# Kernel tuning notes

Hardware: AMD Instinct MI355X
Metric: run time of the kernel (lower is better)

## Reference

```python
import jax, jax.numpy as jnp
import numpy as np

B, L, E = 2, 2048, 1024
H = 16
DH = E // H  # head dim for qk and v (dim_qk=dim_v=embed_dim)
HID = 4 * E  # fcn_dim_factor * dim_v
SCALE = DH ** 0.5


def setup_inputs() -> dict:
    key = jax.random.key(0)
    ks = jax.random.split(key, 12)
    s = lambda fan_in: 1.0 / np.sqrt(fan_in)
    return {
        "x": jax.random.uniform(ks[0], (B, L), jnp.float32),
        "z": jax.random.normal(ks[1], (B, L, E), jnp.float32),
        "Wq": jax.random.normal(ks[2], (E, E), jnp.float32) * s(E),
        "bq": jnp.zeros((E,), jnp.float32),
        "Wk": jax.random.normal(ks[3], (E, E), jnp.float32) * s(E),
        "bk": jnp.zeros((E,), jnp.float32),
        "Wv": jax.random.normal(ks[4], (E, E), jnp.float32) * s(E),
        "bv": jnp.zeros((E,), jnp.float32),
        "W1": jax.random.normal(ks[5], (E, HID), jnp.float32) * s(E),
        "b1": jnp.zeros((HID,), jnp.float32),
        "W2": jax.random.normal(ks[6], (HID, 1), jnp.float32) * s(HID),
        "b2": jnp.zeros((1,), jnp.float32),
    }


def reference(x, z, Wq, bq, Wk, bk, Wv, bv, W1, b1, W2, b2):
    # Projections -> (B, H, L, DH)
    def heads(t):
        return t.reshape(B, L, H, DH).transpose(0, 2, 1, 3)

    Q = heads(z @ Wq + bq)
    K = heads(z @ Wk + bk)
    V = heads(z @ Wv + bv)

    # Scores (B, H, L, L)
    S = jnp.einsum("bhid,bhjd->bhij", Q, K) / SCALE

    # Weighted softmax along query axis (dim=-2), weighted by population x
    w = x[:, None, :, None]  # (B, 1, L, 1), broadcasts over queries i
    m = jnp.max(S, axis=-2, keepdims=True)
    e = w * jnp.exp(S - m)
    A = e / jnp.sum(e, axis=-2, keepdims=True)

    # V scaled by population weight, then AV
    V_scaled = w * V
    O = jnp.einsum("bhij,bhjd->bhid", A, V_scaled)  # (B, H, L, DH)
    O = O.transpose(0, 2, 1, 3).reshape(B, L, H * DH)

    # FFN: Linear -> GELU (exact) -> Linear(->1) -> squeeze
    y = jax.nn.gelu(O @ W1 + b1, approximate=False)
    y = (y @ W2 + b2).squeeze(-1)  # (B, L)
    return y
```

## Files before the change

### kernel.cpp

```cpp
#include <hip/hip_runtime.h>
#include <hip/hip_bf16.h>
#include <math.h>

#define B_    2
#define L_    2048
#define E_    1024
#define H_    16
#define DH_   64
#define HID_  4096
#define NROW_ (B_*L_)
#define BH_   (B_*H_)

#define QSCL  0.18033688011112042f

typedef __attribute__((ext_vector_type(8)))  short    short8v;
typedef _Float16 half8v __attribute__((ext_vector_type(8)));
typedef __attribute__((ext_vector_type(16))) float    f32x16;

#define MFMA32(A, Bv, C) __builtin_amdgcn_mfma_f32_32x32x16_bf16((A), (Bv), (C), 0, 0, 0)
#define MFMAH(A, Bv, C)  __builtin_amdgcn_mfma_f32_32x32x16_f16((A), (Bv), (C), 0, 0, 0)

#define WAITV(N) asm volatile("s_waitcnt vmcnt(" #N ")" ::: "memory")
#define SBAR()   __builtin_amdgcn_s_barrier()

__device__ __forceinline__ unsigned short f2bf(float f) {
    union { float f; unsigned u; } v; v.f = f;
    return (unsigned short)((v.u + 0x8000u) >> 16);
}
__device__ __forceinline__ unsigned pack2_bf16(float lo, float hi) {
    union { float f; unsigned u; } a, b; a.f = lo; b.f = hi;
    return __builtin_amdgcn_perm(b.u + 0x8000u, a.u + 0x8000u, 0x07060302u);
}
__device__ __forceinline__ float bf2f(unsigned short u) {
    union { unsigned u; float f; } v; v.u = ((unsigned)u) << 16;
    return v.f;
}

__device__ __forceinline__ void gl_lds16(const void* g, void* l) {
    __builtin_amdgcn_global_load_lds(
        (const __attribute__((address_space(1))) unsigned int*)g,
        (__attribute__((address_space(3))) unsigned int*)l, 16, 0, 0);
}

__device__ __forceinline__ float erf_fast(float v) {
    float a = fabsf(v);
    float t = __builtin_amdgcn_rcpf(1.0f + 0.3275911f * a);
    float p = t * (0.254829592f + t * (-0.284496736f + t * (1.421413741f +
              t * (-1.453152027f + t * 1.061405429f))));
    float r = 1.0f - p * __expf(-a * a);
    return copysignf(r, v);
}

__global__ __launch_bounds__(256) void zh_prep(
    const float* __restrict__ z, _Float16* __restrict__ zh)
{
    const size_t i = ((size_t)blockIdx.x * 256 + threadIdx.x) * 8;
    float4 a = *(const float4*)&z[i];
    float4 b = *(const float4*)&z[i + 4];
    union { _Float16 h[8]; half8v v; } o;
    o.h[0] = (_Float16)a.x; o.h[1] = (_Float16)a.y;
    o.h[2] = (_Float16)a.z; o.h[3] = (_Float16)a.w;
    o.h[4] = (_Float16)b.x; o.h[5] = (_Float16)b.y;
    o.h[6] = (_Float16)b.z; o.h[7] = (_Float16)b.w;
    *(half8v*)&zh[i] = o.v;
}

__global__ __launch_bounds__(256) void wprep3(
    const float* __restrict__ Wq, const float* __restrict__ Wk,
    const float* __restrict__ Wv,
    _Float16* __restrict__ Tq, _Float16* __restrict__ Tk,
    _Float16* __restrict__ Tv)
{
    const float* src = (blockIdx.z == 0) ? Wq : (blockIdx.z == 1) ? Wk : Wv;
    _Float16*    dst = (blockIdx.z == 0) ? Tq : (blockIdx.z == 1) ? Tk : Tv;
    __shared__ float tile[64][65];
    const int t  = threadIdx.x;
    const int r0 = blockIdx.y * 64, c0 = blockIdx.x * 64;
    #pragma unroll
    for (int u = 0; u < 4; ++u) {
        int f = t + 256 * u, row = f >> 4, c4 = (f & 15) << 2;
        *(float4*)&tile[row][c4] = *(const float4*)&src[(size_t)(r0 + row) * E_ + c0 + c4];
    }
    __syncthreads();
    #pragma unroll
    for (int u = 0; u < 4; ++u) {
        int f = t + 256 * u, c = f >> 4, r4 = (f & 15) << 2;
        union { _Float16 h[4]; uint2 u2; } pk;
        pk.h[0] = (_Float16)tile[r4 + 0][c];
        pk.h[1] = (_Float16)tile[r4 + 1][c];
        pk.h[2] = (_Float16)tile[r4 + 2][c];
        pk.h[3] = (_Float16)tile[r4 + 3][c];
        *(uint2*)&dst[(size_t)(c0 + c) * E_ + r0 + r4] = pk.u2;
    }
}

__global__ __launch_bounds__(256) void w1prep(
    const float* __restrict__ W1, _Float16* __restrict__ W1t)
{
    __shared__ float tile[64][65];
    const int t  = threadIdx.x;
    const int r0 = blockIdx.y * 64, c0 = blockIdx.x * 64;
    #pragma unroll
    for (int u = 0; u < 4; ++u) {
        int f = t + 256 * u, row = f >> 4, c4 = (f & 15) << 2;
        *(float4*)&tile[row][c4] = *(const float4*)&W1[(size_t)(r0 + row) * HID_ + c0 + c4];
    }
    __syncthreads();
    #pragma unroll
    for (int u = 0; u < 4; ++u) {
        int f = t + 256 * u, c = f >> 4, r4 = (f & 15) << 2;
        union { _Float16 h[4]; uint2 u2; } pk;
        pk.h[0] = (_Float16)tile[r4 + 0][c];
        pk.h[1] = (_Float16)tile[r4 + 1][c];
        pk.h[2] = (_Float16)tile[r4 + 2][c];
        pk.h[3] = (_Float16)tile[r4 + 3][c];
        *(uint2*)&W1t[(size_t)(c0 + c) * E_ + r0 + r4] = pk.u2;
    }
}

__global__ __launch_bounds__(256) void qkv_mfma(
    const _Float16* __restrict__ zh,
    const _Float16* __restrict__ Tall,
    const float* __restrict__ bq, const float* __restrict__ bk,
    const float* __restrict__ bv,
    unsigned short* __restrict__ outQKV)
{
    const int which = blockIdx.y >> 3;
    const float* bias = (which == 0) ? bq : (which == 1) ? bk : bv;
    const float  osc  = (which == 0) ? QSCL : 1.0f;
    unsigned short* out = outQKV + (size_t)which * ((size_t)BH_ * L_ * DH_);

    __shared__ _Float16 Ah[2][128 * 64];
    __shared__ _Float16 Bs[2][128 * 64];

    const int t    = threadIdx.x;
    const int lane = t & 63;
    const int w    = t >> 6;
    const int l31  = lane & 31;
    const int hq   = lane >> 5;
    const int wm   = w >> 1, wn = w & 1;
    const int m0   = blockIdx.x * 128;
    const int n0   = blockIdx.y * 128;

    const int srow0 = (lane >> 3);
    const int ssl   = lane & 7;

    f32x16 acc[2][2] = {};

#define QKV_STAGE(bb, kc)                                                          \
    {                                                                              \
        _Pragma("unroll")                                                          \
        for (int u = 0; u < 4; ++u) {                                              \
            int ch  = w * 4 + u;                                                   \
            int row = ch * 8 + srow0;                                              \
            gl_lds16(&zh[(size_t)(m0 + row) * E_ + (kc) * 64 + ((ssl ^ (row & 7)) << 3)], \
                     &Ah[bb][ch * 512]);                                           \
            gl_lds16(&Tall[(size_t)(n0 + row) * E_ + (kc) * 64 + ((ssl ^ (row & 7)) << 3)], \
                     &Bs[bb][ch * 512]);                                           \
        }                                                                          \
    }

    QKV_STAGE(0, 0);
    QKV_STAGE(1, 1);
    __syncthreads();
    int cur = 0;

    for (int kc = 0; kc < 16; ++kc) {
        if (kc < 15) WAITV(8); else WAITV(0);
        SBAR();
        __builtin_amdgcn_s_setprio(1);
        #pragma unroll
        for (int ks = 0; ks < 4; ++ks) {
            half8v fb[2];
            #pragma unroll
            for (int nb = 0; nb < 2; ++nb) {
                int br = wn * 64 + nb * 32 + l31;
                fb[nb] = *(const half8v*)&Bs[cur][br * 64 + (((ks * 2 + hq) ^ (br & 7)) << 3)];
            }
            #pragma unroll
            for (int mb = 0; mb < 2; ++mb) {
                int ar = wm * 64 + mb * 32 + l31;
                half8v fa = *(const half8v*)&Ah[cur][ar * 64 + (((ks * 2 + hq) ^ (ar & 7)) << 3)];
                acc[mb][0] = MFMAH(fa, fb[0], acc[mb][0]);
                acc[mb][1] = MFMAH(fa, fb[1], acc[mb][1]);
            }
        }
        __builtin_amdgcn_s_setprio(0);
        SBAR();
        if (kc + 2 < 16) QKV_STAGE(cur, kc + 2);
        cur ^= 1;
    }

    #pragma unroll
    for (int nb = 0; nb < 2; ++nb) {
        int n  = n0 + wn * 64 + nb * 32 + l31;
        int nn = n & 1023;
        int h  = nn >> 6, dh = nn & 63;
        float bb = bias[nn];
        #pragma unroll
        for (int mb = 0; mb < 2; ++mb) {
            #pragma unroll
            for (int r = 0; r < 16; ++r) {
                int m  = m0 + wm * 64 + mb * 32 + (r & 3) + 8 * (r >> 2) + 4 * hq;
                int b  = m >> 11, i = m & (L_ - 1);
                out[((size_t)(b * H_ + h) * L_ + i) * DH_ + dh] = f2bf((acc[mb][nb][r] + bb) * osc);
            }
        }
    }
#undef QKV_STAGE
}

__global__ __launch_bounds__(512) void col_stats_mfma(
    const unsigned short* __restrict__ Qb, const unsigned short* __restrict__ Kb,
    const float* __restrict__ x, float* __restrict__ Do)
{
    __shared__ unsigned short Qlds[2][2][128 * 64];
    __shared__ float xlds[L_];
    __shared__ float cD[4][64];

    const int t    = threadIdx.x;
    const int lane = t & 63;
    const int wv   = t >> 6;
    const int jwv  = wv & 3;
    const int ih   = wv >> 2;
    const int l31  = lane & 31;
    const int hq   = lane >> 5;
    const int bh   = blockIdx.y;
    const int b    = bh >> 4;
    const int j0   = blockIdx.x * 256 + jwv * 64;

    const int srow0 = (lane >> 3);
    const int ssl   = lane & 7;

    {
        *(float4*)&xlds[t * 4] = *(const float4*)&x[(size_t)b * L_ + t * 4];
    }

    short8v kf[2][4];
    #pragma unroll
    for (int s = 0; s < 2; ++s) {
        const unsigned short* kp = Kb + ((size_t)bh * L_ + j0 + s * 32 + l31) * DH_ + hq * 8;
        #pragma unroll
        for (int c = 0; c < 4; ++c) kf[s][c] = *(const short8v*)(kp + c * 16);
    }

    float d0[16], d1[16];
    #pragma unroll
    for (int r = 0; r < 16; ++r) { d0[r] = 0.f; d1[r] = 0.f; }

#define CS_STAGE(bb, lt)                                                            \
    {                                                                               \
        _Pragma("unroll")                                                           \
        for (int u = 0; u < 4; ++u) {                                               \
            int ch  = jwv * 4 + u;                                                  \
            int row = ch * 8 + srow0;                                               \
            gl_lds16(&Qb[((size_t)bh * L_ + (size_t)(ih * 8 + (lt)) * 128 + row) * DH_ + ((ssl ^ (row & 7)) << 3)], \
                     &Qlds[ih][bb][ch * 512]);                                      \
        }                                                                           \
    }

    CS_STAGE(0, 0);
    CS_STAGE(1, 1);
    __syncthreads();
    int cur = 0;

    for (int lt = 0; lt < 8; ++lt) {
        if (lt < 7) WAITV(4); else WAITV(0);
        SBAR();
        #pragma unroll
        for (int cc = 0; cc < 4; ++cc) {
            f32x16 a0 = {}, a1 = {};
            __builtin_amdgcn_s_setprio(1);
            #pragma unroll
            for (int c = 0; c < 4; ++c) {
                int qr = cc * 32 + l31;
                short8v qv = *(const short8v*)&Qlds[ih][cur][qr * 64 + (((c * 2 + hq) ^ (qr & 7)) << 3)];
                a0 = MFMA32(kf[0][c], qv, a0);
                a1 = MFMA32(kf[1][c], qv, a1);
            }
            __builtin_amdgcn_s_setprio(0);
            float xi = xlds[(ih * 8 + lt) * 128 + cc * 32 + l31];
            #pragma unroll
            for (int r = 0; r < 16; ++r) {
                d0[r] += xi * __builtin_amdgcn_exp2f(a0[r]);
                d1[r] += xi * __builtin_amdgcn_exp2f(a1[r]);
            }
        }
        SBAR();
        if (lt + 2 < 8) CS_STAGE(cur, lt + 2);
        cur ^= 1;
    }

    #pragma unroll
    for (int r = 0; r < 16; ++r) {
        #pragma unroll
        for (int off = 16; off > 0; off >>= 1) {
            d0[r] += __shfl_xor(d0[r], off);
            d1[r] += __shfl_xor(d1[r], off);
        }
    }
    if (ih == 1 && l31 == 0) {
        #pragma unroll
        for (int r = 0; r < 16; ++r) {
            int jr = 4 * hq + (r & 3) + 8 * (r >> 2);
            cD[jwv][jr]      = d0[r];
            cD[jwv][32 + jr] = d1[r];
        }
    }
    __syncthreads();
    if (ih == 0 && l31 == 0) {
        #pragma unroll
        for (int r = 0; r < 16; ++r) {
            int jr = 4 * hq + (r & 3) + 8 * (r >> 2);
            Do[(size_t)bh * L_ + j0 + jr]      = d0[r] + cD[jwv][jr];
            Do[(size_t)bh * L_ + j0 + 32 + jr] = d1[r] + cD[jwv][32 + jr];
        }
    }
#undef CS_STAGE
}

__global__ __launch_bounds__(256) void vt_prep(
    const unsigned short* __restrict__ Vb, const float* __restrict__ x,
    const float* __restrict__ Do, unsigned short* __restrict__ Vt)
{
    __shared__ float sc[64];
    __shared__ unsigned short vt[64][66];

    const int t  = threadIdx.x;
    const int bh = blockIdx.y;
    const int b  = bh >> 4;
    const int j0 = blockIdx.x * 64;

    if (t < 64) {
        int j = j0 + t;
        sc[t] = x[(size_t)b * L_ + j] / Do[(size_t)bh * L_ + j];
    }
    __syncthreads();

    #pragma unroll
    for (int u = 0; u < 2; ++u) {
        int idx = t + 256 * u;
        int row = idx >> 3, off = (idx & 7) * 8;
        short8v v = *(const short8v*)&Vb[((size_t)bh * L_ + j0 + row) * DH_ + off];
        float s = sc[row];
        const unsigned short* vs = (const unsigned short*)&v;
        #pragma unroll
        for (int k = 0; k < 8; ++k)
            vt[row][off + k] = f2bf(bf2f(vs[k]) * s);
    }
    __syncthreads();

    #pragma unroll
    for (int u = 0; u < 2; ++u) {
        int idx = t + 256 * u;
        int dh = idx >> 3, js = (idx & 7) * 8;
        unsigned short o[8];
        #pragma unroll
        for (int k = 0; k < 8; ++k) o[k] = vt[js + k][dh];
        *(short8v*)&Vt[((size_t)bh * DH_ + dh) * L_ + j0 + js] = *(const short8v*)o;
    }
}

__global__ __launch_bounds__(512) void attn_out_mfma(
    const unsigned short* __restrict__ Qb, const unsigned short* __restrict__ Kb,
    const unsigned short* __restrict__ Vt, const float* __restrict__ x,
    _Float16* __restrict__ Of)
{
    __shared__ unsigned short Klds[2][2][64 * 64];
    __shared__ unsigned short Vlds[2][2][64 * 64];
    __shared__ float comb[4][64 * 67];

    const int t    = threadIdx.x;
    const int lane = t & 63;
    const int wv   = t >> 6;
    const int iwv  = wv & 3;
    const int jh   = wv >> 2;
    const int l31  = lane & 31;
    const int hq   = lane >> 5;
    const int bh   = blockIdx.y;
    const int b    = bh >> 4, hh = bh & 15;
    const int iw   = blockIdx.x * 256 + iwv * 64;

    const int srow0 = (lane >> 3);
    const int ssl   = lane & 7;

    short8v qf[2][4];
    #pragma unroll
    for (int ig = 0; ig < 2; ++ig) {
        const unsigned short* qp = Qb + ((size_t)bh * L_ + iw + ig * 32 + l31) * DH_ + hq * 8;
        #pragma unroll
        for (int c = 0; c < 4; ++c) qf[ig][c] = *(const short8v*)(qp + c * 16);
    }

    f32x16 accO[2][2] = {};

#define AO_STAGE(bb, jt)                                                            \
    {                                                                               \
        _Pragma("unroll")                                                           \
        for (int u = 0; u < 2; ++u) {                                               \
            int ch  = iwv * 2 + u;                                                  \
            int row = ch * 8 + srow0;                                               \
            gl_lds16(&Kb[((size_t)bh * L_ + (jt) * 64 + row) * DH_ + ((ssl ^ (row & 7)) << 3)], \
                     &Klds[jh][bb][ch * 512]);                                      \
            gl_lds16(&Vt[((size_t)bh * DH_ + row) * L_ + (jt) * 64 + ((ssl ^ (row & 7)) << 3)], \
                     &Vlds[jh][bb][ch * 512]);                                      \
        }                                                                           \
    }

    AO_STAGE(0, jh * 16 + 0);
    AO_STAGE(1, jh * 16 + 1);
    __syncthreads();
    int cur = 0;

    for (int ltj = 0; ltj < 16; ++ltj) {
        if (ltj < 15) WAITV(4); else WAITV(0);
        SBAR();

        uint4 pa[2][4];
        #pragma unroll
        for (int js = 0; js < 2; ++js) {
            f32x16 as0 = {}, as1 = {};
            __builtin_amdgcn_s_setprio(1);
            #pragma unroll
            for (int c = 0; c < 4; ++c) {
                int krow = js * 32 + l31;
                short8v kfr = *(const short8v*)&Klds[jh][cur][krow * 64 + (((c * 2 + hq) ^ (krow & 7)) << 3)];
                as0 = MFMA32(kfr, qf[0][c], as0);
                as1 = MFMA32(kfr, qf[1][c], as1);
            }
            __builtin_amdgcn_s_setprio(0);
            #pragma unroll
            for (int ig = 0; ig < 2; ++ig) {
                const f32x16& as = (ig == 0) ? as0 : as1;
                float p[16];
                #pragma unroll
                for (int r = 0; r < 16; ++r) p[r] = __builtin_amdgcn_exp2f(as[r]);

                unsigned P0 = pack2_bf16(p[0], p[1]);
                unsigned P1 = pack2_bf16(p[2], p[3]);
                unsigned Q0 = pack2_bf16(p[4], p[5]);
                unsigned Q1 = pack2_bf16(p[6], p[7]);
                asm("v_permlane32_swap_b32 %0, %1" : "+v"(P0), "+v"(Q0));
                asm("v_permlane32_swap_b32 %0, %1" : "+v"(P1), "+v"(Q1));
                pa[ig][js * 2 + 0] = make_uint4(P0, P1, Q0, Q1);

                unsigned R0 = pack2_bf16(p[8],  p[9]);
                unsigned R1 = pack2_bf16(p[10], p[11]);
                unsigned S0 = pack2_bf16(p[12], p[13]);
                unsigned S1 = pack2_bf16(p[14], p[15]);
                asm("v_permlane32_swap_b32 %0, %1" : "+v"(R0), "+v"(S0));
                asm("v_permlane32_swap_b32 %0, %1" : "+v"(R1), "+v"(S1));
                pa[ig][js * 2 + 1] = make_uint4(R0, R1, S0, S1);
            }
        }

        __builtin_amdgcn_s_setprio(1);
        #pragma unroll
        for (int c = 0; c < 4; ++c) {
            union { uint4 u; short8v s; } pa0, pa1;
            pa0.u = pa[0][c]; pa1.u = pa[1][c];
            int r0 = l31, r1 = 32 + l31;
            short8v vf0 = *(const short8v*)&Vlds[jh][cur][r0 * 64 + (((c * 2 + hq) ^ (r0 & 7)) << 3)];
            short8v vf1 = *(const short8v*)&Vlds[jh][cur][r1 * 64 + (((c * 2 + hq) ^ (r1 & 7)) << 3)];
            accO[0][0] = MFMA32(pa0.s, vf0, accO[0][0]);
            accO[0][1] = MFMA32(pa0.s, vf1, accO[0][1]);
            accO[1][0] = MFMA32(pa1.s, vf0, accO[1][0]);
            accO[1][1] = MFMA32(pa1.s, vf1, accO[1][1]);
        }
        __builtin_amdgcn_s_setprio(0);
        SBAR();
        if (ltj + 2 < 16) AO_STAGE(cur, jh * 16 + ltj + 2);
        cur ^= 1;
    }

    if (jh == 1) {
        float* cb = &comb[iwv][lane * 67];
        #pragma unroll
        for (int g = 0; g < 2; ++g)
            #pragma unroll
            for (int h = 0; h < 2; ++h)
                #pragma unroll
                for (int r = 0; r < 16; ++r)
                    cb[(g * 2 + h) * 16 + r] = accO[g][h][r];
    }
    __syncthreads();
    if (jh == 0) {
        const float* cb = &comb[iwv][lane * 67];
        #pragma unroll
        for (int g = 0; g < 2; ++g)
            #pragma unroll
            for (int h = 0; h < 2; ++h)
                #pragma unroll
                for (int r = 0; r < 16; ++r)
                    accO[g][h][r] += cb[(g * 2 + h) * 16 + r];

        #pragma unroll
        for (int ig = 0; ig < 2; ++ig) {
            #pragma unroll
            for (int q = 0; q < 4; ++q) {
                float4 xq = *(const float4*)&x[(size_t)b * L_ + iw + ig * 32 + 4 * hq + 8 * q];
                const float xs[4] = { xq.x, xq.y, xq.z, xq.w };
                #pragma unroll
                for (int k = 0; k < 4; ++k) {
                    int r    = q * 4 + k;
                    int irow = iw + ig * 32 + 4 * hq + 8 * q + k;
                    size_t base = ((size_t)b * L_ + irow) * E_ + hh * DH_;
                    Of[base + l31]      = (_Float16)(accO[ig][0][r] * xs[k]);
                    Of[base + 32 + l31] = (_Float16)(accO[ig][1][r] * xs[k]);
                }
            }
        }
    }
#undef AO_STAGE
}

__global__ __launch_bounds__(256) void mlp_mfma(
    const _Float16* __restrict__ Of, const _Float16* __restrict__ W1t,
    const float* __restrict__ b1, const float* __restrict__ W2,
    const float* __restrict__ b2, float* __restrict__ y)
{
    __shared__ _Float16 Oh[2][128 * 64];
    __shared__ _Float16 Wh[2][128 * 64];

    const int t    = threadIdx.x;
    const int lane = t & 63;
    const int w    = t >> 6;
    const int l31  = lane & 31;
    const int hq   = lane >> 5;
    const int wm   = w >> 1, wn = w & 1;
    const int m0   = blockIdx.x * 128;
    const int n0   = blockIdx.y * 128;

    const int srow0 = (lane >> 3);
    const int ssl   = lane & 7;

    f32x16 acc[2][2] = {};

#define MLP_STAGE(bb, kc)                                                          \
    {                                                                              \
        _Pragma("unroll")                                                          \
        for (int u = 0; u < 4; ++u) {                                              \
            int ch  = w * 4 + u;                                                   \
            int row = ch * 8 + srow0;                                              \
            gl_lds16(&Of[(size_t)(m0 + row) * E_ + (kc) * 64 + ((ssl ^ (row & 7)) << 3)], \
                     &Oh[bb][ch * 512]);                                           \
            gl_lds16(&W1t[(size_t)(n0 + row) * E_ + (kc) * 64 + ((ssl ^ (row & 7)) << 3)], \
                     &Wh[bb][ch * 512]);                                           \
        }                                                                          \
    }

    MLP_STAGE(0, 0);
    MLP_STAGE(1, 1);
    __syncthreads();
    int cur = 0;

    for (int kc = 0; kc < 16; ++kc) {
        if (kc < 15) WAITV(8); else WAITV(0);
        SBAR();
        __builtin_amdgcn_s_setprio(1);
        #pragma unroll
        for (int ks = 0; ks < 4; ++ks) {
            half8v fb[2];
            #pragma unroll
            for (int nb = 0; nb < 2; ++nb) {
                int br = wn * 64 + nb * 32 + l31;
                fb[nb] = *(const half8v*)&Wh[cur][br * 64 + (((ks * 2 + hq) ^ (br & 7)) << 3)];
            }
            #pragma unroll
            for (int mb = 0; mb < 2; ++mb) {
                int ar = wm * 64 + mb * 32 + l31;
                half8v fa = *(const half8v*)&Oh[cur][ar * 64 + (((ks * 2 + hq) ^ (ar & 7)) << 3)];
                acc[mb][0] = MFMAH(fa, fb[0], acc[mb][0]);
                acc[mb][1] = MFMAH(fa, fb[1], acc[mb][1]);
            }
        }
        __builtin_amdgcn_s_setprio(0);
        SBAR();
        if (kc + 2 < 16) MLP_STAGE(cur, kc + 2);
        cur ^= 1;
    }

    const int hid0 = n0 + wn * 64 + l31;
    const float bb0 = b1[hid0],      w20 = W2[hid0];
    const float bb1 = b1[hid0 + 32], w21 = W2[hid0 + 32];
    const float b2v = (blockIdx.y == 0) ? b2[0] : 0.0f;
    #pragma unroll
    for (int mb = 0; mb < 2; ++mb) {
        #pragma unroll
        for (int r = 0; r < 16; ++r) {
            float h0 = acc[mb][0][r] + bb0;
            float h1 = acc[mb][1][r] + bb1;
            float s  = 0.5f * h0 * (1.0f + erf_fast(h0 * 0.70710678f)) * w20
                     + 0.5f * h1 * (1.0f + erf_fast(h1 * 0.70710678f)) * w21;
            #pragma unroll
            for (int off = 16; off > 0; off >>= 1) s += __shfl_xor(s, off);
            if (l31 == 0) {
                int m = m0 + wm * 64 + mb * 32 + (r & 3) + 8 * (r >> 2) + 4 * hq;
                atomicAdd(&y[m], s + b2v);
            }
        }
    }
#undef MLP_STAGE
}

extern "C" void kernel_launch(void* const* d_in, const int* in_sizes, int n_in,
                              void* d_out, int out_size, void* d_ws, size_t ws_size,
                              hipStream_t stream)
{
    const float* x  = (const float*)d_in[0];
    const float* z  = (const float*)d_in[1];
    const float* Wq = (const float*)d_in[2];
    const float* bq = (const float*)d_in[3];
    const float* Wk = (const float*)d_in[4];
    const float* bk = (const float*)d_in[5];
    const float* Wv = (const float*)d_in[6];
    const float* bv = (const float*)d_in[7];
    const float* W1 = (const float*)d_in[8];
    const float* b1 = (const float*)d_in[9];
    const float* W2 = (const float*)d_in[10];
    const float* b2 = (const float*)d_in[11];
    float* y = (float*)d_out;

    const size_t NQ = (size_t)BH_ * L_ * DH_;
    unsigned short* p = (unsigned short*)d_ws;
    unsigned short* Qb  = p;  p += NQ;
    unsigned short* Kb  = p;  p += NQ;
    unsigned short* Vb  = p;  p += NQ;
    unsigned short* Vt  = p;  p += NQ;
    _Float16* zh  = (_Float16*)p;  p += (size_t)NROW_ * E_;
    _Float16* Tq  = (_Float16*)p;  p += (size_t)E_ * E_;
    _Float16* Tk  = (_Float16*)p;  p += (size_t)E_ * E_;
    _Float16* Tv  = (_Float16*)p;  p += (size_t)E_ * E_;
    _Float16* W1t = (_Float16*)p;  p += (size_t)HID_ * E_;
    _Float16* Ofp = (_Float16*)p;  p += (size_t)NROW_ * E_;
    float* Dw = (float*)p;

    hipMemsetAsync(y, 0, (size_t)out_size * sizeof(float), stream);

    zh_prep<<<dim3((NROW_ * E_) / (256 * 8)), 256, 0, stream>>>(z, zh);
    wprep3 <<<dim3(E_ / 64, E_ / 64, 3), 256, 0, stream>>>(Wq, Wk, Wv, Tq, Tk, Tv);
    w1prep <<<dim3(HID_ / 64, E_ / 64), 256, 0, stream>>>(W1, W1t);

    qkv_mfma<<<dim3(NROW_ / 128, 3 * E_ / 128), 256, 0, stream>>>(
        zh, Tq, bq, bk, bv, Qb);

    col_stats_mfma<<<dim3(L_ / 256, BH_), 512, 0, stream>>>(Qb, Kb, x, Dw);

    vt_prep<<<dim3(L_ / 64, BH_), 256, 0, stream>>>(Vb, x, Dw, Vt);

    attn_out_mfma<<<dim3(L_ / 256, BH_), 512, 0, stream>>>(Qb, Kb, Vt, x, Ofp);

    mlp_mfma<<<dim3(NROW_ / 128, HID_ / 128), 256, 0, stream>>>(
        Ofp, W1t, b1, W2, b2, y);
}
```

Measured before the change: 204.8 us.

## Fuse V-transpose prep into column-stats kernel and swap grid axes for locality

The column-softmax denominator kernel now also computes the per-key scale x/D in shared memory and writes the scaled, transposed V tile itself. This removes the separate vt_prep launch and the global round-trip of the denominator buffer. In addition, grid dimensions of the QKV, column-stats, attention and MLP kernels are swapped so that consecutive blocks share the same row tile or head. That ordering is meant to improve L2 reuse of the shared operand. The fused epilogue reuses the Q staging LDS and adds barriers and tail work to the stats kernel.

```diff
diff --git a/kernel.cpp b/kernel.cpp
--- a/kernel.cpp
+++ b/kernel.cpp
@@ -125,7 +125,7 @@
     const float* __restrict__ bv,
     unsigned short* __restrict__ outQKV)
 {
-    const int which = blockIdx.y >> 3;
+    const int which = blockIdx.x >> 3;
     const float* bias = (which == 0) ? bq : (which == 1) ? bk : bv;
     const float  osc  = (which == 0) ? QSCL : 1.0f;
     unsigned short* out = outQKV + (size_t)which * ((size_t)BH_ * L_ * DH_);
@@ -139,8 +139,8 @@
     const int l31  = lane & 31;
     const int hq   = lane >> 5;
     const int wm   = w >> 1, wn = w & 1;
-    const int m0   = blockIdx.x * 128;
-    const int n0   = blockIdx.y * 128;
+    const int m0   = blockIdx.y * 128;
+    const int n0   = blockIdx.x * 128;
 
     const int srow0 = (lane >> 3);
     const int ssl   = lane & 7;
@@ -210,13 +210,15 @@
 #undef QKV_STAGE
 }
 
-__global__ __launch_bounds__(512) void col_stats_mfma(
+__global__ __launch_bounds__(512) void col_stats_vt(
     const unsigned short* __restrict__ Qb, const unsigned short* __restrict__ Kb,
-    const float* __restrict__ x, float* __restrict__ Do)
+    const unsigned short* __restrict__ Vb, const float* __restrict__ x,
+    unsigned short* __restrict__ Vt)
 {
     __shared__ unsigned short Qlds[2][2][128 * 64];
     __shared__ float xlds[L_];
     __shared__ float cD[4][64];
+    __shared__ float sc[256];
 
     const int t    = threadIdx.x;
     const int lane = t & 63;
@@ -225,16 +227,15 @@
     const int ih   = wv >> 2;
     const int l31  = lane & 31;
     const int hq   = lane >> 5;
-    const int bh   = blockIdx.y;
+    const int bh   = blockIdx.x;
     const int b    = bh >> 4;
-    const int j0   = blockIdx.x * 256 + jwv * 64;
+    const int jc0  = blockIdx.y * 256;
+    const int j0   = jc0 + jwv * 64;
 
     const int srow0 = (lane >> 3);
     const int ssl   = lane & 7;
 
-    {
-        *(float4*)&xlds[t * 4] = *(const float4*)&x[(size_t)b * L_ + t * 4];
-    }
+    *(float4*)&xlds[t * 4] = *(const float4*)&x[(size_t)b * L_ + t * 4];
 
     short8v kf[2][4];
     #pragma unroll
@@ -312,53 +313,45 @@
         #pragma unroll
         for (int r = 0; r < 16; ++r) {
             int jr = 4 * hq + (r & 3) + 8 * (r >> 2);
-            Do[(size_t)bh * L_ + j0 + jr]      = d0[r] + cD[jwv][jr];
-            Do[(size_t)bh * L_ + j0 + 32 + jr] = d1[r] + cD[jwv][32 + jr];
+            float D0 = d0[r] + cD[jwv][jr];
+            float D1 = d1[r] + cD[jwv][32 + jr];
+            sc[jwv * 64 + jr]      = xlds[j0 + jr]      / D0;
+            sc[jwv * 64 + 32 + jr] = xlds[j0 + 32 + jr] / D1;
+        }
+    }
+
+    unsigned short (*vtb)[66] = (unsigned short(*)[66])&Qlds[0][0][0];
+    const int half = t >> 8;
+    const int tl   = t & 255;
+    #pragma unroll
+    for (int it = 0; it < 2; ++it) {
+        int tt = it * 2 + half;
+        int jb = jc0 + tt * 64;
+        unsigned short (*vbuf)[66] = vtb + half * 64;
+        __syncthreads();
+        #pragma unroll
+        for (int u = 0; u < 2; ++u) {
+            int idx = tl + 256 * u;
+            int row = idx >> 3, off = (idx & 7) * 8;
+            short8v v = *(const short8v*)&Vb[((size_t)bh * L_ + jb + row) * DH_ + off];
+            float s = sc[tt * 64 + row];
+            const unsigned short* vs = (const unsigned short*)&v;
+            #pragma unroll
+            for (int k = 0; k < 8; ++k)
+                vbuf[row][off + k] = f2bf(bf2f(vs[k]) * s);
+        }
+        __syncthreads();
+        #pragma unroll
+        for (int u = 0; u < 2; ++u) {
+            int idx = tl + 256 * u;
+            int dh = idx >> 3, js = (idx & 7) * 8;
+            unsigned short o[8];
+            #pragma unroll
+            for (int k = 0; k < 8; ++k) o[k] = vbuf[js + k][dh];
+            *(short8v*)&Vt[((size_t)bh * DH_ + dh) * L_ + jb + js] = *(const short8v*)o;
         }
     }
 #undef CS_STAGE
-}
-
-__global__ __launch_bounds__(256) void vt_prep(
-    const unsigned short* __restrict__ Vb, const float* __restrict__ x,
-    const float* __restrict__ Do, unsigned short* __restrict__ Vt)
-{
-    __shared__ float sc[64];
-    __shared__ unsigned short vt[64][66];
-
-    const int t  = threadIdx.x;
-    const int bh = blockIdx.y;
-    const int b  = bh >> 4;
-    const int j0 = blockIdx.x * 64;
-
-    if (t < 64) {
-        int j = j0 + t;
-        sc[t] = x[(size_t)b * L_ + j] / Do[(size_t)bh * L_ + j];
-    }
-    __syncthreads();
-
-    #pragma unroll
-    for (int u = 0; u < 2; ++u) {
-        int idx = t + 256 * u;
-        int row = idx >> 3, off = (idx & 7) * 8;
-        short8v v = *(const short8v*)&Vb[((size_t)bh * L_ + j0 + row) * DH_ + off];
-        float s = sc[row];
-        const unsigned short* vs = (const unsigned short*)&v;
-        #pragma unroll
-        for (int k = 0; k < 8; ++k)
-            vt[row][off + k] = f2bf(bf2f(vs[k]) * s);
-    }
-    __syncthreads();
-
-    #pragma unroll
-    for (int u = 0; u < 2; ++u) {
-        int idx = t + 256 * u;
-        int dh = idx >> 3, js = (idx & 7) * 8;
-        unsigned short o[8];
-        #pragma unroll
-        for (int k = 0; k < 8; ++k) o[k] = vt[js + k][dh];
-        *(short8v*)&Vt[((size_t)bh * DH_ + dh) * L_ + j0 + js] = *(const short8v*)o;
-    }
 }
 
 __global__ __launch_bounds__(512) void attn_out_mfma(
@@ -377,9 +370,9 @@
     const int jh   = wv >> 2;
     const int l31  = lane & 31;
     const int hq   = lane >> 5;
-    const int bh   = blockIdx.y;
+    const int bh   = blockIdx.x;
     const int b    = bh >> 4, hh = bh & 15;
-    const int iw   = blockIdx.x * 256 + iwv * 64;
+    const int iw   = blockIdx.y * 256 + iwv * 64;
 
     const int srow0 = (lane >> 3);
     const int ssl   = lane & 7;
@@ -528,8 +521,8 @@
     const int l31  = lane & 31;
     const int hq   = lane >> 5;
     const int wm   = w >> 1, wn = w & 1;
-    const int m0   = blockIdx.x * 128;
-    const int n0   = blockIdx.y * 128;
+    const int m0   = blockIdx.y * 128;
+    const int n0   = blockIdx.x * 128;
 
     const int srow0 = (lane >> 3);
     const int ssl   = lane & 7;
@@ -583,7 +576,7 @@
     const int hid0 = n0 + wn * 64 + l31;
     const float bb0 = b1[hid0],      w20 = W2[hid0];
     const float bb1 = b1[hid0 + 32], w21 = W2[hid0 + 32];
-    const float b2v = (blockIdx.y == 0) ? b2[0] : 0.0f;
+    const float b2v = (blockIdx.x == 0) ? b2[0] : 0.0f;
     #pragma unroll
     for (int mb = 0; mb < 2; ++mb) {
         #pragma unroll
@@ -633,7 +626,6 @@
     _Float16* Tv  = (_Float16*)p;  p += (size_t)E_ * E_;
     _Float16* W1t = (_Float16*)p;  p += (size_t)HID_ * E_;
     _Float16* Ofp = (_Float16*)p;  p += (size_t)NROW_ * E_;
-    float* Dw = (float*)p;
 
     hipMemsetAsync(y, 0, (size_t)out_size * sizeof(float), stream);
 
@@ -641,15 +633,13 @@
     wprep3 <<<dim3(E_ / 64, E_ / 64, 3), 256, 0, stream>>>(Wq, Wk, Wv, Tq, Tk, Tv);
     w1prep <<<dim3(HID_ / 64, E_ / 64), 256, 0, stream>>>(W1, W1t);
 
-    qkv_mfma<<<dim3(NROW_ / 128, 3 * E_ / 128), 256, 0, stream>>>(
+    qkv_mfma<<<dim3(3 * E_ / 128, NROW_ / 128), 256, 0, stream>>>(
         zh, Tq, bq, bk, bv, Qb);
 
-    col_stats_mfma<<<dim3(L_ / 256, BH_), 512, 0, stream>>>(Qb, Kb, x, Dw);
-
-    vt_prep<<<dim3(L_ / 64, BH_), 256, 0, stream>>>(Vb, x, Dw, Vt);
-
-    attn_out_mfma<<<dim3(L_ / 256, BH_), 512, 0, stream>>>(Qb, Kb, Vt, x, Ofp);
-
-    mlp_mfma<<<dim3(NROW_ / 128, HID_ / 128), 256, 0, stream>>>(
+    col_stats_vt<<<dim3(BH_, L_ / 256), 512, 0, stream>>>(Qb, Kb, Vb, x, Vt);
+
+    attn_out_mfma<<<dim3(BH_, L_ / 256), 512, 0, stream>>>(Qb, Kb, Vt, x, Ofp);
+
+    mlp_mfma<<<dim3(HID_ / 128, NROW_ / 128), 256, 0, stream>>>(
         Ofp, W1t, b1, W2, b2, y);
 }
```

Measured after the change: 211.3 us. +3.2%, slower.
